# Performance work log

Hardware: AMD Instinct MI355X
Metric: run time of the kernel (lower is better)

The kernel has to match this reference:

```python
import jax, jax.numpy as jnp
import numpy as np

N_NODES = 100000
N_EDGES = 3200000
N_FEAT = 128
EMB = 64
HID = 64
N_SUB = 500000
N_GRAPHS = 1024
BN_EPS = 1e-5


def setup_inputs() -> dict:
    key = jax.random.key(0)
    ks = jax.random.split(key, 12)
    full_x = jax.random.normal(ks[0], (N_NODES, N_FEAT), dtype=jnp.float32)
    full_edge_index = jax.random.randint(ks[1], (2, N_EDGES), 0, N_NODES, dtype=jnp.int64)
    subgraph_node_indices = jax.random.randint(ks[2], (N_SUB,), 0, N_NODES, dtype=jnp.int64)
    batch_vector = jax.random.randint(ks[3], (N_SUB,), 0, N_GRAPHS, dtype=jnp.int64)
    # GCNConv params (glorot-style scale)
    W_enc = jax.random.normal(ks[4], (N_FEAT, EMB), dtype=jnp.float32) * (1.0 / np.sqrt(N_FEAT))
    b_enc = jnp.zeros((EMB,), dtype=jnp.float32)
    # predictor MLP params
    W1 = jax.random.normal(ks[5], (EMB, HID), dtype=jnp.float32) * (1.0 / np.sqrt(EMB))
    b1 = jnp.zeros((HID,), dtype=jnp.float32)
    gamma = jnp.ones((HID,), dtype=jnp.float32)
    beta = jnp.zeros((HID,), dtype=jnp.float32)
    W2 = jax.random.normal(ks[6], (HID, 1), dtype=jnp.float32) * (1.0 / np.sqrt(HID))
    b2 = jnp.zeros((1,), dtype=jnp.float32)
    return {
        "full_x": full_x,
        "full_edge_index": full_edge_index,
        "subgraph_node_indices": subgraph_node_indices,
        "batch_vector": batch_vector,
        "W_enc": W_enc, "b_enc": b_enc,
        "W1": W1, "b1": b1, "gamma": gamma, "beta": beta,
        "W2": W2, "b2": b2,
    }


def gcn_conv(x, edge_index, W, b):
    # PyG GCNConv: add self-loops, symmetric degree normalization, linear transform
    n = x.shape[0]
    loops = jnp.arange(n, dtype=edge_index.dtype)
    row = jnp.concatenate([edge_index[0], loops])  # source
    col = jnp.concatenate([edge_index[1], loops])  # target
    deg = jax.ops.segment_sum(jnp.ones_like(col, dtype=x.dtype), col, num_segments=n)
    dinv = jnp.where(deg > 0, jax.lax.rsqrt(deg), 0.0)
    norm = dinv[row] * dinv[col]  # [E+N]
    xw = x @ W  # transform first: [N, EMB]
    msgs = xw[row] * norm[:, None]
    out = jax.ops.segment_sum(msgs, col, num_segments=n)
    return out + b


def reference(full_x, full_edge_index, subgraph_node_indices, batch_vector,
              W_enc, b_enc, W1, b1, gamma, beta, W2, b2):
    # encoder + relu over all nodes
    h = jax.nn.relu(gcn_conv(full_x, full_edge_index, W_enc, b_enc))  # [N, EMB]
    # gather subgraph members
    sub = h[subgraph_node_indices]  # [N_SUB, EMB]
    # segment-mean pool into per-subgraph embeddings
    sums = jax.ops.segment_sum(sub, batch_vector, num_segments=N_GRAPHS)
    cnts = jax.ops.segment_sum(jnp.ones((sub.shape[0],), sub.dtype), batch_vector, num_segments=N_GRAPHS)
    pooled = sums / jnp.maximum(cnts, 1.0)[:, None]  # [N_GRAPHS, EMB]
    # predictor: Linear -> ReLU -> BatchNorm1d (training-mode batch stats) -> Linear
    z = jax.nn.relu(pooled @ W1 + b1)  # [N_GRAPHS, HID]
    mu = jnp.mean(z, axis=0)
    var = jnp.mean((z - mu) ** 2, axis=0)  # biased, as torch BN normalization
    zn = (z - mu) * jax.lax.rsqrt(var + BN_EPS) * gamma + beta
    return zn @ W2 + b2  # [N_GRAPHS, 1]
```

## Files before the change

kernel.cpp:

```cpp
#include <hip/hip_runtime.h>

#define N_NODES 100000
#define N_EDGES 3200000
#define N_FEAT 128
#define EMB 64
#define HID 64
#define N_SUB 500000
#define N_GRAPHS 1024
#define BN_EPS 1e-5f

#define NBKT 782
#define TILE 4096
#define NTILES 782
#define NGTILES 123
#define BKT_MAX 4864
#define GCAP 640
#define ZROW 100000

typedef __attribute__((ext_vector_type(8))) short short8;
typedef __attribute__((ext_vector_type(4))) float floatx4;

#define OFF_BCUR   0u
#define OFF_BCURG  4096u
#define OFF_BNSUM  8192u
#define ZERO_BYTES 8704u
#define OFF_DINV   12288u
#define OFF_OFFS   412672u
#define OFF_PAIRS  812672u
#define OFF_XWS    OFF_PAIRS
#define OFF_CSR    16027264u
#define OFF_SORTED 31241856u
#define OFF_H      33863296u
#define OFF_Z      46676608u

__device__ __forceinline__ bool is_bf(const unsigned* gamma_raw) {
  return (gamma_raw[0] & 0xFFFFu) != 0u;
}
__device__ __forceinline__ bool idx_is64(const int* subp) {
  return (subp[1] | subp[3] | subp[5] | subp[7]) == 0;
}
__device__ __forceinline__ int ld_idx(const int* p, long long i, bool w64) {
  return w64 ? p[2 * i] : p[i];
}
__device__ __forceinline__ float bf2f(ushort u) {
  union { unsigned i; float f; } v; v.i = ((unsigned)u) << 16; return v.f;
}
__device__ __forceinline__ ushort f2bf(float f) {
  union { float f; unsigned i; } v; v.f = f;
  unsigned lsb = (v.i >> 16) & 1u;
  v.i += 0x7FFFu + lsb;
  return (ushort)(v.i >> 16);
}
__device__ __forceinline__ float ld_f(const void* p, int i, bool bf) {
  return bf ? bf2f(((const ushort*)p)[i]) : ((const float*)p)[i];
}
__device__ __forceinline__ float lo_bf(unsigned d) {
  union { unsigned u; float f; } v; v.u = d << 16; return v.f;
}
__device__ __forceinline__ float hi_bf(unsigned d) {
  union { unsigned u; float f; } v; v.u = d & 0xFFFF0000u; return v.f;
}

__global__ void k_scatsort(const int* e, const int* subp, const int* batch,
                           int* bcur, unsigned* pairs, int* bcurg, int* sorted) {
  __shared__ char smem[36896];
  int* cnt   = (int*)smem;
  int* lscan = cnt + 1024;
  int* gbase = lscan + 1024;
  int* wsum  = gbase + 1024;
  unsigned* stage = (unsigned*)(wsum + 8);
  unsigned short* stgb = (unsigned short*)(stage + 4096);
  bool w64 = idx_is64(subp);
  int tid = threadIdx.x, lane = tid & 63, wv = tid >> 6;
  bool edges = blockIdx.x < NTILES;
  int nb   = edges ? NBKT : N_GRAPHS;
  int base = edges ? blockIdx.x * TILE : (blockIdx.x - NTILES) * TILE;
  int tot  = edges ? N_EDGES : N_SUB;
  int tcnt = min(TILE, tot - base);
  for (int i = tid; i < nb; i += 512) cnt[i] = 0;
  __syncthreads();
  if (edges) {
    if (w64) {
      const int2* tp = (const int2*)e + (size_t)N_EDGES + base;
      for (int j = tid; j < tcnt; j += 512) atomicAdd(&cnt[tp[j].x >> 7], 1);
    } else {
      for (int j = tid; j < tcnt; j += 512)
        atomicAdd(&cnt[e[N_EDGES + base + j] >> 7], 1);
    }
  } else {
    if (w64) {
      const int2* bp = (const int2*)batch + base;
      for (int j = tid; j < tcnt; j += 512) atomicAdd(&cnt[bp[j].x], 1);
    } else {
      for (int j = tid; j < tcnt; j += 512) atomicAdd(&cnt[batch[base + j]], 1);
    }
  }
  __syncthreads();
  int b0 = tid * 2, v0 = 0, v1 = 0, s = 0;
  if (b0 < nb) {
    v0 = cnt[b0];
    v1 = (b0 + 1 < nb) ? cnt[b0 + 1] : 0;
    s = v0 + v1;
  }
  int val = s;
#pragma unroll
  for (int d = 1; d < 64; d <<= 1) {
    int t = __shfl_up(val, d);
    if (lane >= d) val += t;
  }
  if (lane == 63) wsum[wv] = val;
  __syncthreads();
  int woff = 0;
#pragma unroll
  for (int w = 0; w < 8; ++w) woff += (w < wv) ? wsum[w] : 0;
  if (b0 < nb) {
    int excl = (val + woff) - s;
    lscan[b0] = excl;
    if (b0 + 1 < nb) lscan[b0 + 1] = excl + v0;
  }
  __syncthreads();
  for (int b = tid; b < nb; b += 512) {
    int c = cnt[b];
    gbase[b] = c ? (edges ? b * BKT_MAX + atomicAdd(&bcur[b], c)
                          : b * GCAP + atomicAdd(&bcurg[b], c)) : 0;
    cnt[b] = 0;
  }
  __syncthreads();
  if (edges) {
    for (int j = tid; j < tcnt; j += 512) {
      int src, tgt;
      if (w64) {
        src = ((const int2*)e)[base + j].x;
        tgt = ((const int2*)e)[(size_t)N_EDGES + base + j].x;
      } else {
        src = e[base + j];
        tgt = e[N_EDGES + base + j];
      }
      int b = tgt >> 7;
      int r = atomicAdd(&cnt[b], 1);
      int p = lscan[b] + r;
      stage[p] = ((unsigned)(tgt & 127) << 20) | (unsigned)src;
      stgb[p] = (unsigned short)b;
    }
  } else {
    for (int j = tid; j < tcnt; j += 512) {
      int g, nid;
      if (w64) {
        g = ((const int2*)batch)[base + j].x;
        nid = ((const int2*)subp)[base + j].x;
      } else {
        g = batch[base + j];
        nid = subp[base + j];
      }
      int r = atomicAdd(&cnt[g], 1);
      int p = lscan[g] + r;
      stage[p] = (unsigned)nid;
      stgb[p] = (unsigned short)g;
    }
  }
  __syncthreads();
  if (edges) {
    for (int j = tid; j < tcnt; j += 512) {
      int b = stgb[j];
      pairs[gbase[b] + (j - lscan[b])] = stage[j];
    }
  } else {
    for (int j = tid; j < tcnt; j += 512) {
      int b = stgb[j];
      sorted[gbase[b] + (j - lscan[b])] = (int)stage[j];
    }
  }
}

__global__ void k_csr(const unsigned* __restrict__ pairs, const int* __restrict__ bcur,
                      int* __restrict__ csr, unsigned* __restrict__ offs,
                      float* __restrict__ dinv) {
  __shared__ int dl[128], loff[128], lcur[128];
  __shared__ int stage[BKT_MAX];
  int tid = threadIdx.x, b = blockIdx.x;
  if (tid < 128) dl[tid] = 0;
  __syncthreads();
  int s = b * BKT_MAX, cnt = bcur[b];
  {
    int j = tid;
    unsigned pn = (j < cnt) ? pairs[s + j] : 0u;
    for (; j < cnt; j += 512) {
      unsigned p = pn;
      int jn = j + 512;
      pn = (jn < cnt) ? pairs[s + jn] : 0u;
      atomicAdd(&dl[p >> 20], 1);
    }
  }
  __syncthreads();
  if (tid < 128) loff[tid] = dl[tid];
  __syncthreads();
  for (int d = 1; d < 128; d <<= 1) {
    int t = (tid >= d && tid < 128) ? loff[tid - d] : 0;
    __syncthreads();
    if (tid < 128) loff[tid] += t;
    __syncthreads();
  }
  if (tid < 128) {
    int deg = dl[tid];
    int excl = loff[tid] - deg;
    lcur[tid] = excl;
    int n = b * 128 + tid;
    if (n < N_NODES) {
      offs[n] = ((unsigned)deg << 24) | (unsigned)(s + excl);
      dinv[n] = rsqrtf((float)(deg + 1));
    }
  }
  __syncthreads();
  {
    int j = tid;
    unsigned pn = (j < cnt) ? pairs[s + j] : 0u;
    for (; j < cnt; j += 512) {
      unsigned p = pn;
      int jn = j + 512;
      pn = (jn < cnt) ? pairs[s + jn] : 0u;
      int pos = atomicAdd(&lcur[p >> 20], 1);
      stage[pos] = (int)(p & 0xFFFFF);
    }
  }
  __syncthreads();
  for (int j = tid; j < cnt; j += 512) csr[s + j] = stage[j];
}

__global__ void k_gemm(const void* xraw, const void* Wraw, const unsigned* gamu,
                       const float* __restrict__ dinv, ushort* __restrict__ xws) {
  if (blockIdx.x == 0 && threadIdx.x < 32)
    ((unsigned*)xws)[(unsigned)ZROW * 32u + threadIdx.x] = 0u;
  bool bf = is_bf(gamu);
  const ushort* Wus = (const ushort*)Wraw;
  const float*  Wf  = (const float*)Wraw;
  int wv = threadIdx.x >> 6, lane = threadIdx.x & 63;
  int m = lane & 15, quad = lane >> 4;
  int c0 = wv * 16;
  short8 bfrag[4];
#pragma unroll
  for (int kc = 0; kc < 4; ++kc)
#pragma unroll
    for (int j = 0; j < 8; ++j) {
      int idx = (kc * 32 + quad * 8 + j) * EMB + c0 + m;
      bfrag[kc][j] = (short)(bf ? Wus[idx] : f2bf(Wf[idx]));
    }
  const ushort* xs = (const ushort*)xraw;
  const float*  xf = (const float*)xraw;
  for (int t = blockIdx.x; t < N_NODES / 16; t += gridDim.x) {
    int r0 = t * 16;
    floatx4 acc = {0.f, 0.f, 0.f, 0.f};
    if (bf) {
#pragma unroll
      for (int kc = 0; kc < 4; ++kc) {
        short8 a = *(const short8*)(xs + (r0 + m) * N_FEAT + kc * 32 + quad * 8);
        acc = __builtin_amdgcn_mfma_f32_16x16x32_bf16(a, bfrag[kc], acc, 0, 0, 0);
      }
    } else {
#pragma unroll
      for (int kc = 0; kc < 4; ++kc) {
        const float* ap = xf + (r0 + m) * N_FEAT + kc * 32 + quad * 8;
        float4 f0 = *(const float4*)ap, f1 = *(const float4*)(ap + 4);
        short8 a;
        a[0] = (short)f2bf(f0.x); a[1] = (short)f2bf(f0.y);
        a[2] = (short)f2bf(f0.z); a[3] = (short)f2bf(f0.w);
        a[4] = (short)f2bf(f1.x); a[5] = (short)f2bf(f1.y);
        a[6] = (short)f2bf(f1.z); a[7] = (short)f2bf(f1.w);
        acc = __builtin_amdgcn_mfma_f32_16x16x32_bf16(a, bfrag[kc], acc, 0, 0, 0);
      }
    }
#pragma unroll
    for (int r = 0; r < 4; ++r) {
      int row = r0 + quad * 4 + r;
      xws[row * EMB + c0 + m] = f2bf(acc[r] * dinv[row]);
    }
  }
}

#define ACCU(d) { aL0 += lo_bf(d.x); aH0 += hi_bf(d.x); aL1 += lo_bf(d.y); aH1 += hi_bf(d.y); \
                  aL2 += lo_bf(d.z); aH2 += hi_bf(d.z); aL3 += lo_bf(d.w); aH3 += hi_bf(d.w); }

__global__ void k_agg(const ushort* __restrict__ xws, const float* __restrict__ dinv,
                      const unsigned* __restrict__ offs, const int* __restrict__ csr,
                      const void* benc, const unsigned* gamu, ushort* __restrict__ h) {
  if (blockIdx.x == 0 && threadIdx.x < 32)
    ((unsigned*)h)[(unsigned)ZROW * 32u + threadIdx.x] = 0u;
  bool bf = is_bf(gamu);
  const uint4* xw4 = (const uint4*)xws;
  int wv = threadIdx.x >> 6, lane = threadIdx.x & 63;
  int e8 = lane >> 3, q = lane & 7;
  int n = blockIdx.x * 4 + wv;
  unsigned w = offs[n];
  int start = (int)(w & 0xFFFFFFu), end = start + (int)(w >> 24);
  float aL0 = 0.f, aH0 = 0.f, aL1 = 0.f, aH1 = 0.f, aL2 = 0.f, aH2 = 0.f, aL3 = 0.f, aH3 = 0.f;
  for (int i = start; i < end; i += 32) {
    int i0 = i + e8, i1 = i0 + 8, i2 = i0 + 16, i3 = i0 + 24;
    int l0 = csr[i0], l1 = csr[i1], l2 = csr[i2], l3 = csr[i3];
    int s0 = (i0 < end) ? l0 : ZROW;
    int s1 = (i1 < end) ? l1 : ZROW;
    int s2 = (i2 < end) ? l2 : ZROW;
    int s3 = (i3 < end) ? l3 : ZROW;
    uint4 u0 = xw4[s0 * 8 + q];
    uint4 u1 = xw4[s1 * 8 + q];
    uint4 u2 = xw4[s2 * 8 + q];
    uint4 u3 = xw4[s3 * 8 + q];
    ACCU(u0) ACCU(u1) ACCU(u2) ACCU(u3)
  }
#pragma unroll
  for (int msk = 8; msk < 64; msk <<= 1) {
    aL0 += __shfl_xor(aL0, msk); aH0 += __shfl_xor(aH0, msk);
    aL1 += __shfl_xor(aL1, msk); aH1 += __shfl_xor(aH1, msk);
    aL2 += __shfl_xor(aL2, msk); aH2 += __shfl_xor(aH2, msk);
    aL3 += __shfl_xor(aL3, msk); aH3 += __shfl_xor(aH3, msk);
  }
  if (e8 == 0) {
    float dn = dinv[n];
    uint4 us = xw4[n * 8 + q];
    ushort o[8];
    o[0] = f2bf(fmaxf((aL0 + lo_bf(us.x)) * dn + ld_f(benc, q * 8 + 0, bf), 0.f));
    o[1] = f2bf(fmaxf((aH0 + hi_bf(us.x)) * dn + ld_f(benc, q * 8 + 1, bf), 0.f));
    o[2] = f2bf(fmaxf((aL1 + lo_bf(us.y)) * dn + ld_f(benc, q * 8 + 2, bf), 0.f));
    o[3] = f2bf(fmaxf((aH1 + hi_bf(us.y)) * dn + ld_f(benc, q * 8 + 3, bf), 0.f));
    o[4] = f2bf(fmaxf((aL2 + lo_bf(us.z)) * dn + ld_f(benc, q * 8 + 4, bf), 0.f));
    o[5] = f2bf(fmaxf((aH2 + hi_bf(us.z)) * dn + ld_f(benc, q * 8 + 5, bf), 0.f));
    o[6] = f2bf(fmaxf((aL3 + lo_bf(us.w)) * dn + ld_f(benc, q * 8 + 6, bf), 0.f));
    o[7] = f2bf(fmaxf((aH3 + hi_bf(us.w)) * dn + ld_f(benc, q * 8 + 7, bf), 0.f));
    uint4 ov;
    ov.x = (unsigned)o[0] | ((unsigned)o[1] << 16);
    ov.y = (unsigned)o[2] | ((unsigned)o[3] << 16);
    ov.z = (unsigned)o[4] | ((unsigned)o[5] << 16);
    ov.w = (unsigned)o[6] | ((unsigned)o[7] << 16);
    ((uint4*)h)[n * 8 + q] = ov;
  }
}

__global__ void k_poolmlp1(const ushort* __restrict__ h, const int* __restrict__ sorted,
                           const int* __restrict__ bcurg, const void* W1, const void* b1,
                           const unsigned* gamu, float* __restrict__ z, float* bn) {
  bool bf = is_bf(gamu);
  __shared__ float red[4 * 64];
  __shared__ float pl[64];
  const uint4* h4 = (const uint4*)h;
  int g = blockIdx.x;
  int tid = threadIdx.x, wv = tid >> 6, lane = tid & 63;
  int e8 = lane >> 3, q = lane & 7;
  int start = g * GCAP, cnt = bcurg[g];
  int end = start + cnt;
  float aL0 = 0.f, aH0 = 0.f, aL1 = 0.f, aH1 = 0.f, aL2 = 0.f, aH2 = 0.f, aL3 = 0.f, aH3 = 0.f;
  for (int i = start + wv * 32; i < end; i += 128) {
#pragma unroll
    for (int c = 0; c < 4; ++c) {
      int idx = i + c * 8 + e8;
      int l = sorted[idx];
      int nn = (idx < end) ? l : ZROW;
      uint4 u = h4[nn * 8 + q];
      ACCU(u)
    }
  }
#pragma unroll
  for (int msk = 8; msk < 64; msk <<= 1) {
    aL0 += __shfl_xor(aL0, msk); aH0 += __shfl_xor(aH0, msk);
    aL1 += __shfl_xor(aL1, msk); aH1 += __shfl_xor(aH1, msk);
    aL2 += __shfl_xor(aL2, msk); aH2 += __shfl_xor(aH2, msk);
    aL3 += __shfl_xor(aL3, msk); aH3 += __shfl_xor(aH3, msk);
  }
  if (e8 == 0) {
    float* r = red + wv * 64 + q * 8;
    r[0] = aL0; r[1] = aH0; r[2] = aL1; r[3] = aH1;
    r[4] = aL2; r[5] = aH2; r[6] = aL3; r[7] = aH3;
  }
  __syncthreads();
  if (tid < 64) {
    float s = red[tid] + red[64 + tid] + red[128 + tid] + red[192 + tid];
    pl[tid] = s / fmaxf((float)cnt, 1.f);
  }
  __syncthreads();
  if (tid < 64) {
    int f = tid;
    float acc = ld_f(b1, f, bf);
#pragma unroll 8
    for (int k = 0; k < HID; ++k) acc += pl[k] * ld_f(W1, k * HID + f, bf);
    float zv = fmaxf(acc, 0.f);
    z[g * HID + f] = zv;
    atomicAdd(&bn[f], zv);
    atomicAdd(&bn[HID + f], zv * zv);
  }
}

__global__ void k_mlp2(const float* __restrict__ z, const float* __restrict__ bn,
                       const void* gmm, const void* beta, const void* W2, const void* b2,
                       const unsigned* gamu, void* out) {
  bool bf = is_bf(gamu);
  int wv = threadIdx.x >> 6, f = threadIdx.x & 63;
  int g = blockIdx.x * 4 + wv;
  float mu = bn[f] * (1.f / N_GRAPHS);
  float var = bn[HID + f] * (1.f / N_GRAPHS) - mu * mu;
  float zn = (z[g * HID + f] - mu) * rsqrtf(var + BN_EPS) * ld_f(gmm, f, bf) + ld_f(beta, f, bf);
  float val = zn * ld_f(W2, f, bf);
  for (int off = 32; off; off >>= 1) val += __shfl_down(val, off);
  if (f == 0) {
    val += ld_f(b2, 0, bf);
    if (bf) ((ushort*)out)[g] = f2bf(val);
    else    ((float*)out)[g]  = val;
  }
}

extern "C" void kernel_launch(void* const* d_in, const int* in_sizes, int n_in,
                              void* d_out, int out_size, void* d_ws, size_t ws_size,
                              hipStream_t stream) {
  const void* x_raw    = d_in[0];
  const int*  e_raw    = (const int*)d_in[1];
  const int*  sub_raw  = (const int*)d_in[2];
  const int*  bat_raw  = (const int*)d_in[3];
  const void* Wenc     = d_in[4];
  const void* benc     = d_in[5];
  const void* W1       = d_in[6];
  const void* b1       = d_in[7];
  const unsigned* gamu = (const unsigned*)d_in[8];
  const void* beta     = d_in[9];
  const void* W2       = d_in[10];
  const void* b2       = d_in[11];

  char* ws = (char*)d_ws;
  int*      bcur   = (int*)(ws + OFF_BCUR);
  int*      bcurg  = (int*)(ws + OFF_BCURG);
  float*    bnsum  = (float*)(ws + OFF_BNSUM);
  float*    dinv   = (float*)(ws + OFF_DINV);
  unsigned* offs   = (unsigned*)(ws + OFF_OFFS);
  unsigned* pairs  = (unsigned*)(ws + OFF_PAIRS);
  ushort*   xws    = (ushort*)(ws + OFF_XWS);
  int*      csr    = (int*)(ws + OFF_CSR);
  int*      sorted = (int*)(ws + OFF_SORTED);
  ushort*   h      = (ushort*)(ws + OFF_H);
  float*    z      = (float*)(ws + OFF_Z);

  hipMemsetAsync(ws, 0, ZERO_BYTES, stream);

  k_scatsort<<<NTILES + NGTILES, 512, 0, stream>>>(e_raw, sub_raw, bat_raw,
                                                   bcur, pairs, bcurg, sorted);
  k_csr     <<<NBKT, 512, 0, stream>>>(pairs, bcur, csr, offs, dinv);
  k_gemm    <<<1024, 256, 0, stream>>>(x_raw, Wenc, gamu, dinv, xws);
  k_agg     <<<N_NODES / 4, 256, 0, stream>>>(xws, dinv, offs, csr, benc, gamu, h);
  k_poolmlp1<<<N_GRAPHS, 256, 0, stream>>>(h, sorted, bcurg, W1, b1, gamu, z, bnsum);
  k_mlp2    <<<N_GRAPHS / 4, 256, 0, stream>>>(z, bnsum, gamu, beta, W2, b2, gamu, d_out);
}
```

Before: 281.7 us.

## Pad CSR rows to 32, vectorize index loads, register-stage bucket sort

The CSR build now pads each node's neighbour list to a multiple of 32 with the zero-row index. It also keeps the bucket's pairs in registers instead of reading them twice, and writes CSR in place over the pairs buffer. The aggregation kernel then loops a fixed number of iterations and loads four neighbour indices at once as int4, with no per-element bounds checks. The scatter-sort kernel switches to 256 threads that each load 16 keys and values with vector loads up front, then reuse them for the count and scatter passes. The trade-offs are extra padded workspace with a larger bucket capacity, and extra zero-row gathers for the padding slots.

```diff
diff --git a/kernel.cpp b/kernel.cpp
--- a/kernel.cpp
+++ b/kernel.cpp
@@ -13,9 +13,10 @@
 #define TILE 4096
 #define NTILES 782
 #define NGTILES 123
-#define BKT_MAX 4864
+#define BKT_CAP 7168
 #define GCAP 640
 #define ZROW 100000
+#define RPT 9
 
 typedef __attribute__((ext_vector_type(8))) short short8;
 typedef __attribute__((ext_vector_type(4))) float floatx4;
@@ -27,20 +28,17 @@
 #define OFF_DINV   12288u
 #define OFF_OFFS   412672u
 #define OFF_PAIRS  812672u
-#define OFF_XWS    OFF_PAIRS
-#define OFF_CSR    16027264u
-#define OFF_SORTED 31241856u
-#define OFF_H      33863296u
-#define OFF_Z      46676608u
+#define OFF_CSR    OFF_PAIRS
+#define OFF_XWS    23235200u
+#define OFF_SORTED 36035328u
+#define OFF_H      38656768u
+#define OFF_Z      51456896u
 
 __device__ __forceinline__ bool is_bf(const unsigned* gamma_raw) {
   return (gamma_raw[0] & 0xFFFFu) != 0u;
 }
 __device__ __forceinline__ bool idx_is64(const int* subp) {
   return (subp[1] | subp[3] | subp[5] | subp[7]) == 0;
-}
-__device__ __forceinline__ int ld_idx(const int* p, long long i, bool w64) {
-  return w64 ? p[2 * i] : p[i];
 }
 __device__ __forceinline__ float bf2f(ushort u) {
   union { unsigned i; float f; } v; v.i = ((unsigned)u) << 16; return v.f;
@@ -61,138 +59,125 @@
   union { unsigned u; float f; } v; v.u = d & 0xFFFF0000u; return v.f;
 }
 
-__global__ void k_scatsort(const int* e, const int* subp, const int* batch,
-                           int* bcur, unsigned* pairs, int* bcurg, int* sorted) {
-  __shared__ char smem[36896];
-  int* cnt   = (int*)smem;
-  int* lscan = cnt + 1024;
-  int* gbase = lscan + 1024;
-  int* wsum  = gbase + 1024;
-  unsigned* stage = (unsigned*)(wsum + 8);
-  unsigned short* stgb = (unsigned short*)(stage + 4096);
+__global__ __launch_bounds__(256) void k_scatsort(
+    const int* e, const int* subp, const int* batch,
+    int* bcur, unsigned* pairs, int* bcurg, int* sorted) {
+  __shared__ int cnt[1024], lscan[1024], gbase[1024], wsum[4];
+  __shared__ unsigned stage[TILE];
+  __shared__ unsigned short stgb[TILE];
   bool w64 = idx_is64(subp);
   int tid = threadIdx.x, lane = tid & 63, wv = tid >> 6;
   bool edges = blockIdx.x < NTILES;
-  int nb   = edges ? NBKT : N_GRAPHS;
   int base = edges ? blockIdx.x * TILE : (blockIdx.x - NTILES) * TILE;
   int tot  = edges ? N_EDGES : N_SUB;
+  int nb   = edges ? NBKT : N_GRAPHS;
   int tcnt = min(TILE, tot - base);
-  for (int i = tid; i < nb; i += 512) cnt[i] = 0;
-  __syncthreads();
-  if (edges) {
+  int key[16], val[16];
+  bool act = tid * 16 < tcnt;
+  const int* kb = edges ? e : batch;
+  const int* vb = edges ? e : subp;
+  long long ko = edges ? (long long)N_EDGES : 0;
+  if (act) {
     if (w64) {
-      const int2* tp = (const int2*)e + (size_t)N_EDGES + base;
-      for (int j = tid; j < tcnt; j += 512) atomicAdd(&cnt[tp[j].x >> 7], 1);
+      const int4* kp = (const int4*)kb + (ko + base) / 2 + tid * 8;
+      const int4* vp = (const int4*)vb + base / 2 + tid * 8;
+#pragma unroll
+      for (int k = 0; k < 8; ++k) {
+        int4 a = kp[k]; key[2 * k] = a.x; key[2 * k + 1] = a.z;
+        int4 c = vp[k]; val[2 * k] = c.x; val[2 * k + 1] = c.z;
+      }
     } else {
-      for (int j = tid; j < tcnt; j += 512)
-        atomicAdd(&cnt[e[N_EDGES + base + j] >> 7], 1);
-    }
-  } else {
-    if (w64) {
-      const int2* bp = (const int2*)batch + base;
-      for (int j = tid; j < tcnt; j += 512) atomicAdd(&cnt[bp[j].x], 1);
-    } else {
-      for (int j = tid; j < tcnt; j += 512) atomicAdd(&cnt[batch[base + j]], 1);
-    }
-  }
-  __syncthreads();
-  int b0 = tid * 2, v0 = 0, v1 = 0, s = 0;
-  if (b0 < nb) {
-    v0 = cnt[b0];
-    v1 = (b0 + 1 < nb) ? cnt[b0 + 1] : 0;
-    s = v0 + v1;
-  }
-  int val = s;
+      const int4* kp = (const int4*)(kb + ko) + base / 4 + tid * 4;
+      const int4* vp = (const int4*)vb + base / 4 + tid * 4;
+#pragma unroll
+      for (int k = 0; k < 4; ++k) {
+        int4 a = kp[k];
+        key[4 * k] = a.x; key[4 * k + 1] = a.y; key[4 * k + 2] = a.z; key[4 * k + 3] = a.w;
+        int4 c = vp[k];
+        val[4 * k] = c.x; val[4 * k + 1] = c.y; val[4 * k + 2] = c.z; val[4 * k + 3] = c.w;
+      }
+    }
+  }
+  for (int i = tid; i < 1024; i += 256) cnt[i] = 0;
+  __syncthreads();
+  if (act) {
+#pragma unroll
+    for (int k = 0; k < 16; ++k)
+      atomicAdd(&cnt[edges ? (key[k] >> 7) : key[k]], 1);
+  }
+  __syncthreads();
+  int b0 = tid * 4;
+  int v0 = cnt[b0], v1 = cnt[b0 + 1], v2 = cnt[b0 + 2], v3 = cnt[b0 + 3];
+  int s = v0 + v1 + v2 + v3, sc = s;
 #pragma unroll
   for (int d = 1; d < 64; d <<= 1) {
-    int t = __shfl_up(val, d);
-    if (lane >= d) val += t;
-  }
-  if (lane == 63) wsum[wv] = val;
+    int t = __shfl_up(sc, d);
+    if (lane >= d) sc += t;
+  }
+  if (lane == 63) wsum[wv] = sc;
   __syncthreads();
   int woff = 0;
 #pragma unroll
-  for (int w = 0; w < 8; ++w) woff += (w < wv) ? wsum[w] : 0;
-  if (b0 < nb) {
-    int excl = (val + woff) - s;
-    lscan[b0] = excl;
-    if (b0 + 1 < nb) lscan[b0 + 1] = excl + v0;
-  }
-  __syncthreads();
-  for (int b = tid; b < nb; b += 512) {
-    int c = cnt[b];
-    gbase[b] = c ? (edges ? b * BKT_MAX + atomicAdd(&bcur[b], c)
+  for (int w = 0; w < 4; ++w) woff += (w < wv) ? wsum[w] : 0;
+  int excl = sc + woff - s;
+  lscan[b0] = excl; lscan[b0 + 1] = excl + v0;
+  lscan[b0 + 2] = excl + v0 + v1; lscan[b0 + 3] = excl + v0 + v1 + v2;
+  __syncthreads();
+  for (int b = tid; b < 1024; b += 256) {
+    int c = (b < nb) ? cnt[b] : 0;
+    gbase[b] = c ? (edges ? b * BKT_CAP + atomicAdd(&bcur[b], c)
                           : b * GCAP + atomicAdd(&bcurg[b], c)) : 0;
-    cnt[b] = 0;
-  }
-  __syncthreads();
-  if (edges) {
-    for (int j = tid; j < tcnt; j += 512) {
-      int src, tgt;
-      if (w64) {
-        src = ((const int2*)e)[base + j].x;
-        tgt = ((const int2*)e)[(size_t)N_EDGES + base + j].x;
-      } else {
-        src = e[base + j];
-        tgt = e[N_EDGES + base + j];
-      }
-      int b = tgt >> 7;
+  }
+  __syncthreads();
+  for (int b = tid; b < 1024; b += 256) cnt[b] = 0;
+  __syncthreads();
+  if (act) {
+#pragma unroll
+    for (int k = 0; k < 16; ++k) {
+      int b = edges ? (key[k] >> 7) : key[k];
       int r = atomicAdd(&cnt[b], 1);
       int p = lscan[b] + r;
-      stage[p] = ((unsigned)(tgt & 127) << 20) | (unsigned)src;
+      stage[p] = edges ? (((unsigned)(key[k] & 127) << 20) | (unsigned)val[k])
+                       : (unsigned)val[k];
       stgb[p] = (unsigned short)b;
     }
-  } else {
-    for (int j = tid; j < tcnt; j += 512) {
-      int g, nid;
-      if (w64) {
-        g = ((const int2*)batch)[base + j].x;
-        nid = ((const int2*)subp)[base + j].x;
-      } else {
-        g = batch[base + j];
-        nid = subp[base + j];
-      }
-      int r = atomicAdd(&cnt[g], 1);
-      int p = lscan[g] + r;
-      stage[p] = (unsigned)nid;
-      stgb[p] = (unsigned short)g;
-    }
   }
   __syncthreads();
   if (edges) {
-    for (int j = tid; j < tcnt; j += 512) {
+    for (int j = tid; j < tcnt; j += 256) {
       int b = stgb[j];
       pairs[gbase[b] + (j - lscan[b])] = stage[j];
     }
   } else {
-    for (int j = tid; j < tcnt; j += 512) {
+    for (int j = tid; j < tcnt; j += 256) {
       int b = stgb[j];
       sorted[gbase[b] + (j - lscan[b])] = (int)stage[j];
     }
   }
 }
 
-__global__ void k_csr(const unsigned* __restrict__ pairs, const int* __restrict__ bcur,
-                      int* __restrict__ csr, unsigned* __restrict__ offs,
-                      float* __restrict__ dinv) {
+__global__ __launch_bounds__(512) void k_csr(
+    const unsigned* __restrict__ pairs, const int* __restrict__ bcur,
+    int* __restrict__ csr, unsigned* __restrict__ offs, float* __restrict__ dinv) {
   __shared__ int dl[128], loff[128], lcur[128];
-  __shared__ int stage[BKT_MAX];
+  __shared__ int stage[BKT_CAP];
+  __shared__ int ptot;
   int tid = threadIdx.x, b = blockIdx.x;
   if (tid < 128) dl[tid] = 0;
   __syncthreads();
-  int s = b * BKT_MAX, cnt = bcur[b];
-  {
-    int j = tid;
-    unsigned pn = (j < cnt) ? pairs[s + j] : 0u;
-    for (; j < cnt; j += 512) {
-      unsigned p = pn;
-      int jn = j + 512;
-      pn = (jn < cnt) ? pairs[s + jn] : 0u;
-      atomicAdd(&dl[p >> 20], 1);
-    }
-  }
-  __syncthreads();
-  if (tid < 128) loff[tid] = dl[tid];
+  int s = b * BKT_CAP, cnt = bcur[b];
+  unsigned pr[RPT];
+#pragma unroll
+  for (int k = 0; k < RPT; ++k) {
+    int j = tid + k * 512;
+    pr[k] = (j < cnt) ? pairs[s + j] : 0u;
+  }
+#pragma unroll
+  for (int k = 0; k < RPT; ++k)
+    if (tid + k * 512 < cnt) atomicAdd(&dl[pr[k] >> 20], 1);
+  __syncthreads();
+  int deg = 0, pd = 0;
+  if (tid < 128) { deg = dl[tid]; pd = (deg + 31) & ~31; loff[tid] = pd; }
   __syncthreads();
   for (int d = 1; d < 128; d <<= 1) {
     int t = (tid >= d && tid < 128) ? loff[tid - d] : 0;
@@ -201,29 +186,28 @@
     __syncthreads();
   }
   if (tid < 128) {
-    int deg = dl[tid];
-    int excl = loff[tid] - deg;
+    int excl = loff[tid] - pd;
     lcur[tid] = excl;
     int n = b * 128 + tid;
     if (n < N_NODES) {
-      offs[n] = ((unsigned)deg << 24) | (unsigned)(s + excl);
+      offs[n] = ((unsigned)(pd >> 5) << 24) | (unsigned)(s + excl);
       dinv[n] = rsqrtf((float)(deg + 1));
     }
-  }
-  __syncthreads();
-  {
-    int j = tid;
-    unsigned pn = (j < cnt) ? pairs[s + j] : 0u;
-    for (; j < cnt; j += 512) {
-      unsigned p = pn;
-      int jn = j + 512;
-      pn = (jn < cnt) ? pairs[s + jn] : 0u;
-      int pos = atomicAdd(&lcur[p >> 20], 1);
-      stage[pos] = (int)(p & 0xFFFFF);
-    }
-  }
-  __syncthreads();
-  for (int j = tid; j < cnt; j += 512) csr[s + j] = stage[j];
+    if (tid == 127) ptot = loff[127];
+  }
+  __syncthreads();
+  int pt = ptot;
+  for (int j = tid; j < pt; j += 512) stage[j] = ZROW;
+  __syncthreads();
+#pragma unroll
+  for (int k = 0; k < RPT; ++k) {
+    if (tid + k * 512 < cnt) {
+      int pos = atomicAdd(&lcur[pr[k] >> 20], 1);
+      stage[pos] = (int)(pr[k] & 0xFFFFF);
+    }
+  }
+  __syncthreads();
+  for (int j = tid; j < pt; j += 512) csr[s + j] = stage[j];
 }
 
 __global__ void k_gemm(const void* xraw, const void* Wraw, const unsigned* gamu,
@@ -290,19 +274,16 @@
   int e8 = lane >> 3, q = lane & 7;
   int n = blockIdx.x * 4 + wv;
   unsigned w = offs[n];
-  int start = (int)(w & 0xFFFFFFu), end = start + (int)(w >> 24);
+  int start = (int)(w & 0xFFFFFFu);
+  int iters = (int)(w >> 24);
   float aL0 = 0.f, aH0 = 0.f, aL1 = 0.f, aH1 = 0.f, aL2 = 0.f, aH2 = 0.f, aL3 = 0.f, aH3 = 0.f;
-  for (int i = start; i < end; i += 32) {
-    int i0 = i + e8, i1 = i0 + 8, i2 = i0 + 16, i3 = i0 + 24;
-    int l0 = csr[i0], l1 = csr[i1], l2 = csr[i2], l3 = csr[i3];
-    int s0 = (i0 < end) ? l0 : ZROW;
-    int s1 = (i1 < end) ? l1 : ZROW;
-    int s2 = (i2 < end) ? l2 : ZROW;
-    int s3 = (i3 < end) ? l3 : ZROW;
-    uint4 u0 = xw4[s0 * 8 + q];
-    uint4 u1 = xw4[s1 * 8 + q];
-    uint4 u2 = xw4[s2 * 8 + q];
-    uint4 u3 = xw4[s3 * 8 + q];
+  const int4* ip = (const int4*)(csr + start) + e8;
+  for (int it = 0; it < iters; ++it) {
+    int4 idx = ip[it * 8];
+    uint4 u0 = xw4[idx.x * 8 + q];
+    uint4 u1 = xw4[idx.y * 8 + q];
+    uint4 u2 = xw4[idx.z * 8 + q];
+    uint4 u3 = xw4[idx.w * 8 + q];
     ACCU(u0) ACCU(u1) ACCU(u2) ACCU(u3)
   }
 #pragma unroll
@@ -427,15 +408,15 @@
   float*    dinv   = (float*)(ws + OFF_DINV);
   unsigned* offs   = (unsigned*)(ws + OFF_OFFS);
   unsigned* pairs  = (unsigned*)(ws + OFF_PAIRS);
+  int*      csr    = (int*)(ws + OFF_CSR);
   ushort*   xws    = (ushort*)(ws + OFF_XWS);
-  int*      csr    = (int*)(ws + OFF_CSR);
   int*      sorted = (int*)(ws + OFF_SORTED);
   ushort*   h      = (ushort*)(ws + OFF_H);
   float*    z      = (float*)(ws + OFF_Z);
 
   hipMemsetAsync(ws, 0, ZERO_BYTES, stream);
 
-  k_scatsort<<<NTILES + NGTILES, 512, 0, stream>>>(e_raw, sub_raw, bat_raw,
+  k_scatsort<<<NTILES + NGTILES, 256, 0, stream>>>(e_raw, sub_raw, bat_raw,
                                                    bcur, pairs, bcurg, sorted);
   k_csr     <<<NBKT, 512, 0, stream>>>(pairs, bcur, csr, offs, dinv);
   k_gemm    <<<1024, 256, 0, stream>>>(x_raw, Wenc, gamu, dinv, xws);
```

After: 280.6 us. Within noise of the previous version (-0.4%).
